# Kernel optimization log

Measured on AMD Instinct MI355X. Metric: run time of the kernel, lower is better.

Reference implementation:

```python
import jax, jax.numpy as jnp
import numpy as np

VOCAB = 50257
K = 10  # accuracy_slack_size


def setup_inputs() -> dict:
    key = jax.random.key(0)
    k1, k2, k3, k4 = jax.random.split(key, 4)
    logits = jax.random.normal(k1, (4, 2048, 512), dtype=jnp.float32)
    target = jax.random.randint(k2, (4, 2048), 0, VOCAB, dtype=jnp.int64 if jax.config.jax_enable_x64 else jnp.int32)
    mask = jax.random.randint(k3, (4, 2048), 0, 2, dtype=jnp.int32)
    W = jax.random.normal(k4, (512, VOCAB), dtype=jnp.float32) * 0.02
    b = jnp.zeros((VOCAB,), dtype=jnp.float32)
    return {"logits": logits, "target": target, "mask": mask, "W": W, "b": b}


def reference(logits, target, mask, W, b):
    N = logits.shape[0] * logits.shape[1]
    x = logits.reshape(N, logits.shape[-1])            # [N, d]
    # sampled_softmax.log_prob: full log-softmax over vocab
    logp = jax.nn.log_softmax(x @ W + b, axis=-1)      # [N, V]
    _, words = jax.lax.top_k(logp, K)                  # [N, K] indices
    tgt = target.reshape(-1)                           # [N]
    msk = mask.reshape(-1).astype(jnp.float32)         # [N]
    # vectorized membership: is target among top-K predictions?
    hit = jnp.any(words == tgt[:, None], axis=1).astype(jnp.float32)
    counter = jnp.sum(hit * msk)
    all_counter = jnp.sum(msk)
    return jnp.array([counter / all_counter])
```

## Files before the change

### kernel.cpp

```cpp
#include <hip/hip_runtime.h>
#include <stdint.h>

#define V_VOCAB 50257
#define V_PAD   51200
#define NROWS   8192
#define DIM     512
#define KTOP    10
#define ACH     16

typedef __attribute__((ext_vector_type(8))) short  short8;
typedef __attribute__((ext_vector_type(4))) float  f32x4;
typedef __attribute__((ext_vector_type(4))) int    i32x4;
typedef __attribute__((ext_vector_type(2))) unsigned int u32x2;

struct Ctrl { int mc; int namb; int hits; int pad_; };

#define OFF_WT8    0ULL
#define SZ_WT8     26214400ULL
#define OFF_XQ8    (OFF_WT8 + SZ_WT8)
#define SZ_XQ8     4194304ULL
#define OFF_BPAD   (OFF_XQ8 + SZ_XQ8)
#define SZ_COL     (51200ULL*4)
#define OFF_SW8    (OFF_BPAD + SZ_COL)
#define OFF_W1     (OFF_SW8 + SZ_COL)
#define OFF_IVW    (OFF_W1 + SZ_COL)
#define OFF_ROWIDX (OFF_IVW + SZ_COL)
#define OFF_SXR    (OFF_ROWIDX + 32768ULL)
#define OFF_X1     (OFF_SXR + 32768ULL)
#define OFF_THAT   (OFF_X1 + 32768ULL)
#define OFF_ETG    (OFF_THAT + 32768ULL)
#define OFF_COUNTS (OFF_ETG + 32768ULL)
#define OFF_AMB    (OFF_COUNTS + 32768ULL)
#define OFF_CTRL   (OFF_AMB + 32768ULL)
#define OFF_RK     (OFF_CTRL + 16ULL)
#define OFF_SST    (OFF_RK + 32768ULL)

#define GLOAD16(gp, lp) __builtin_amdgcn_global_load_lds( \
    (const __attribute__((address_space(1))) unsigned int*)(gp), \
    (__attribute__((address_space(3))) unsigned int*)(lp), 16, 0, 0)

__global__ void k_prep(const int* __restrict__ mask, const float* __restrict__ b,
                       float* __restrict__ bpad, int* __restrict__ rowidx,
                       Ctrl* __restrict__ ctrl) {
  int i = blockIdx.x * 256 + threadIdx.x;
  if (i < V_PAD) bpad[i] = (i < V_VOCAB) ? b[i] : -1e30f;
  if (i < NROWS && mask[i] != 0) {
    int p = atomicAdd(&ctrl->mc, 1);
    rowidx[p] = i;
  }
}

__global__ void k_wstat(const float* __restrict__ W, float* __restrict__ sw8,
                        float* __restrict__ w1, float* __restrict__ invw) {
  const int j = blockIdx.x * 256 + threadIdx.x;
  if (j >= V_PAD) return;
  if (j >= V_VOCAB) { sw8[j] = 1.f; w1[j] = 0.f; invw[j] = 0.f; return; }
  float am = 0.f, s1 = 0.f;
  for (int k = 0; k < DIM; ++k) {
    float v = fabsf(W[(size_t)k * V_VOCAB + j]);
    am = fmaxf(am, v);
    s1 += v;
  }
  sw8[j] = (am > 0.f) ? am / 126.f : 1.f;
  invw[j] = (am > 0.f) ? 126.f / am : 0.f;
  w1[j] = s1;
}

__global__ void k_twt8(const float* __restrict__ W, const float* __restrict__ invw,
                       signed char* __restrict__ Wt8) {
  __shared__ float lt[64][65];
  const int vbase = blockIdx.x * 64;
  const int kbase = blockIdx.y * 64;
  const int tid = threadIdx.x;
  const int krow = tid >> 6;
  const int col  = tid & 63;
  const int v    = vbase + col;
#pragma unroll
  for (int rr = 0; rr < 16; ++rr) {
    int kl = krow + rr * 4;
    float val = (v < V_VOCAB) ? W[(size_t)(kbase + kl) * V_VOCAB + v] : 0.0f;
    lt[kl][col] = val;
  }
  __syncthreads();
  const int vr = tid >> 3;
  const int kc = tid & 7;
#pragma unroll
  for (int p = 0; p < 2; ++p) {
    const int vl = p * 32 + vr;
    const float inv = invw[vbase + vl];
    unsigned int lo = 0, hi = 0;
#pragma unroll
    for (int j = 0; j < 4; ++j) {
      int q = (int)rintf(lt[kc * 8 + j][vl] * inv);
      lo |= ((unsigned int)(q & 255)) << (8 * j);
    }
#pragma unroll
    for (int j = 0; j < 4; ++j) {
      int q = (int)rintf(lt[kc * 8 + 4 + j][vl] * inv);
      hi |= ((unsigned int)(q & 255)) << (8 * j);
    }
    u32x2 t; t.x = lo; t.y = hi;
    *(u32x2*)(Wt8 + (size_t)(vbase + vl) * DIM + kbase + kc * 8) = t;
  }
}

__global__ void k_xq(const float* __restrict__ x, const int* __restrict__ rowidx,
                     const Ctrl* __restrict__ ctrl, signed char* __restrict__ Xq8,
                     float* __restrict__ sxr, float* __restrict__ x1) {
  const int wid = threadIdx.x >> 6, lane = threadIdx.x & 63;
  const int i = blockIdx.x * 4 + wid;
  const int mc = ctrl->mc;
  if (i >= mc) {
    u32x2 z; z.x = 0; z.y = 0;
    *(u32x2*)(Xq8 + (size_t)i * DIM + lane * 8) = z;
    if (lane == 0) { sxr[i] = 1.f; x1[i] = 0.f; }
    return;
  }
  const float* src = x + (size_t)rowidx[i] * DIM + lane * 8;
  float v[8];
  float am = 0.f, s1 = 0.f;
#pragma unroll
  for (int j = 0; j < 8; ++j) {
    v[j] = src[j];
    float a = fabsf(v[j]);
    am = fmaxf(am, a);
    s1 += a;
  }
#pragma unroll
  for (int d = 1; d < 64; d <<= 1) {
    am = fmaxf(am, __shfl_xor(am, d, 64));
    s1 += __shfl_xor(s1, d, 64);
  }
  const float sx  = (am > 0.f) ? am / 126.f : 1.f;
  const float inv = (am > 0.f) ? 126.f / am : 0.f;
  unsigned int lo = 0, hi = 0;
#pragma unroll
  for (int j = 0; j < 4; ++j) {
    int q = (int)rintf(v[j] * inv);
    lo |= ((unsigned int)(q & 255)) << (8 * j);
  }
#pragma unroll
  for (int j = 0; j < 4; ++j) {
    int q = (int)rintf(v[4 + j] * inv);
    hi |= ((unsigned int)(q & 255)) << (8 * j);
  }
  u32x2 t; t.x = lo; t.y = hi;
  *(u32x2*)(Xq8 + (size_t)i * DIM + lane * 8) = t;
  if (lane == 0) { sxr[i] = sx; x1[i] = s1; }
}

__global__ void k_that8(const signed char* __restrict__ Xq8,
                        const signed char* __restrict__ Wt8,
                        const float* __restrict__ bpad, const float* __restrict__ sw8,
                        const float* __restrict__ w1,
                        const float* __restrict__ sxr, const float* __restrict__ x1,
                        const int* __restrict__ rowidx, const int* __restrict__ target,
                        const Ctrl* __restrict__ ctrl, float* __restrict__ that,
                        float* __restrict__ etg) {
  const int wid = threadIdx.x >> 6, lane = threadIdx.x & 63;
  const int i = blockIdx.x * 4 + wid;
  const int mc = ctrl->mc;
  if (i >= mc) { if (lane == 0) { that[i] = 1e30f; etg[i] = 0.f; } return; }
  const int tg = target[rowidx[i]];
  u32x2 xq = *(const u32x2*)(Xq8 + (size_t)i * DIM + lane * 8);
  u32x2 wq = *(const u32x2*)(Wt8 + (size_t)tg * DIM + lane * 8);
  int d = 0;
#pragma unroll
  for (int j = 0; j < 4; ++j)
    d += (int)((signed char)(xq.x >> (8 * j))) * (int)((signed char)(wq.x >> (8 * j)));
#pragma unroll
  for (int j = 0; j < 4; ++j)
    d += (int)((signed char)(xq.y >> (8 * j))) * (int)((signed char)(wq.y >> (8 * j)));
#pragma unroll
  for (int dd = 1; dd < 64; dd <<= 1) d += __shfl_xor(d, dd, 64);
  if (lane == 0) {
    const float sx = sxr[i], sw = sw8[tg];
    that[i] = fmaf((float)d, sx * sw, bpad[tg]);
    etg[i] = 0.5005f * (sx * w1[tg] + sw * x1[i]) + 128.5f * (sx * sw);
  }
}

__launch_bounds__(256, 2)
__global__ void k_count8(const signed char* __restrict__ Xq8,
                         const signed char* __restrict__ Wt8,
                         const float* __restrict__ bpad, const float* __restrict__ sw8,
                         const float* __restrict__ w1, const float* __restrict__ sxr,
                         const float* __restrict__ x1, const float* __restrict__ that,
                         const float* __restrict__ etg,
                         const Ctrl* __restrict__ ctrl, unsigned int* __restrict__ counts) {
  const int mc = ctrl->mc;
  const int lin = blockIdx.x;
  const int xcd = lin & 7;
  const int idx = lin >> 3;
  const int mt  = xcd * 4 + (idx & 3);
  const int nt  = idx >> 2;
  const int mbase = mt * 128;
  if (mbase >= mc) return;
  const int nbase = nt * 128;

  __shared__ char lds[65536];

  const int tid  = threadIdx.x;
  const int lane = tid & 63;
  const int w    = tid >> 6;
  const int wr   = w >> 1;
  const int wc   = w & 1;

  const char* Ag = (const char*)Xq8 + (size_t)mbase * 512;
  const char* Bg = (const char*)Wt8 + (size_t)nbase * 512;
  const int r8   = tid >> 3;
  const int sws  = ((tid & 7) ^ (r8 & 7)) * 16;
  const int dst0 = tid * 16;

  const int fr = lane & 15;
  const int fq = lane >> 4;
  const int p0 = ((fq) ^ (fr & 7)) * 16;
  const int p1 = ((4 + fq) ^ (fr & 7)) * 16;

#define STAGE(q, kt) do {                                                      \
    const size_t _kb = (size_t)(kt) * 128;                                     \
    _Pragma("unroll") for (int _c = 0; _c < 4; ++_c)                           \
      GLOAD16(Ag + (size_t)(_c * 32 + r8) * 512 + _kb + sws,                   \
              lds + (q) * 32768 + _c * 4096 + dst0);                           \
    _Pragma("unroll") for (int _c = 0; _c < 4; ++_c)                           \
      GLOAD16(Bg + (size_t)(_c * 32 + r8) * 512 + _kb + sws,                   \
              lds + (q) * 32768 + 16384 + _c * 4096 + dst0);                   \
  } while (0)

  i32x4 acc[4][4];
#pragma unroll
  for (int a = 0; a < 4; ++a)
#pragma unroll
    for (int c = 0; c < 4; ++c) acc[a][c] = (i32x4)0;

#define KTILE(q) do {                                                          \
    const char* _ab = lds + (q) * 32768;                                       \
    const char* _bb = _ab + 16384;                                             \
    _Pragma("unroll") for (int _ks = 0; _ks < 2; ++_ks) {                      \
      const int _p = _ks ? p1 : p0;                                            \
      i32x4 a4[4], b4[4];                                                      \
      _Pragma("unroll") for (int _i = 0; _i < 4; ++_i)                         \
        a4[_i] = *(const i32x4*)(_ab + (wr * 64 + _i * 16 + fr) * 128 + _p);   \
      _Pragma("unroll") for (int _i = 0; _i < 4; ++_i)                         \
        b4[_i] = *(const i32x4*)(_bb + (wc * 64 + _i * 16 + fr) * 128 + _p);   \
      __builtin_amdgcn_s_setprio(1);                                           \
      _Pragma("unroll") for (int _m = 0; _m < 4; ++_m)                         \
      _Pragma("unroll") for (int _n = 0; _n < 4; ++_n)                         \
        acc[_m][_n] = __builtin_amdgcn_mfma_i32_16x16x64_i8(                   \
            a4[_m], b4[_n], acc[_m][_n], 0, 0, 0);                             \
      __builtin_amdgcn_s_setprio(0);                                           \
    }                                                                          \
  } while (0)

  STAGE(0, 0);
  __syncthreads();
#pragma unroll
  for (int kt = 0; kt < 4; ++kt) {
    if (kt < 3) STAGE((kt + 1) & 1, kt + 1);
    KTILE(kt & 1);
    __syncthreads();
  }

  float bv[4], swc[4], w1c[4];
#pragma unroll
  for (int ni = 0; ni < 4; ++ni) {
    const int c = nbase + wc * 64 + ni * 16 + fr;
    bv[ni] = bpad[c]; swc[ni] = sw8[c]; w1c[ni] = w1[c];
  }

#pragma unroll
  for (int mi = 0; mi < 4; ++mi) {
#pragma unroll
    for (int r = 0; r < 4; ++r) {
      const int m = mbase + wr * 64 + mi * 16 + fq * 4 + r;
      const float sx = sxr[m], x1r = x1[m], th = that[m], eg = etg[m];
      unsigned int p = 0;
#pragma unroll
      for (int ni = 0; ni < 4; ++ni) {
        const float scl = sx * swc[ni];
        const float s = fmaf((float)acc[mi][ni][r], scl, bv[ni]);
        const float mm = 0.5005f * (sx * w1c[ni] + swc[ni] * x1r)
                         + 128.5f * scl + eg + 1e-3f;
        p += (s > th - mm) ? 1u : 0u;
        p += (s > th + mm) ? (1u << 16) : 0u;
      }
      int pi = (int)p;
#pragma unroll
      for (int d = 1; d < 16; d <<= 1) pi += __shfl_xor(pi, d, 64);
      if ((lane & 15) == 0) atomicAdd(&counts[m], (unsigned int)pi);
    }
  }
#undef STAGE
#undef KTILE
}

__global__ void k_decide(const unsigned int* __restrict__ counts,
                         Ctrl* __restrict__ ctrl, int* __restrict__ amb) {
  const int i = blockIdx.x * 256 + threadIdx.x;
  if (i >= ctrl->mc) return;
  const unsigned int c = counts[i];
  const unsigned int lo = c & 0xFFFFu, hi = c >> 16;
  if (lo <= KTOP - 1) { atomicAdd(&ctrl->hits, 1); }
  else if (hi >= KTOP) {  }
  else { int p = atomicAdd(&ctrl->namb, 1); amb[p] = i; }
}

__global__ void k_fixt(const float* __restrict__ x, const float* __restrict__ W,
                       const float* __restrict__ b, const int* __restrict__ rowidx,
                       const int* __restrict__ target, const int* __restrict__ amb,
                       const Ctrl* __restrict__ ctrl, float* __restrict__ sst) {
  const int a = blockIdx.x * 64 + threadIdx.x;
  if (a >= ctrl->namb) return;
  const int n = rowidx[amb[a]];
  const int tg = target[n];
  float st = 0.f;
  for (int k = 0; k < DIM; ++k)
    st = fmaf(x[(size_t)n * DIM + k], W[(size_t)k * V_VOCAB + tg], st);
  sst[a] = st + b[tg];
}

__global__ void k_fixscan(const float* __restrict__ x, const float* __restrict__ W,
                          const float* __restrict__ b, const int* __restrict__ rowidx,
                          const int* __restrict__ target, const int* __restrict__ amb,
                          const float* __restrict__ sst, const Ctrl* __restrict__ ctrl,
                          int* __restrict__ rk) {
  __shared__ float sx[ACH][DIM];
  const int j = blockIdx.x * 256 + threadIdx.x;
  const int namb = ctrl->namb;
  const float bj = (j < V_VOCAB) ? b[j] : 0.f;
  for (int base = 0; base < namb; base += ACH) {
    __syncthreads();
    for (int t = threadIdx.x; t < ACH * DIM / 4; t += 256) {
      const int a  = t / (DIM / 4);
      const int kk = (t % (DIM / 4)) * 4;
      f32x4 v = (f32x4)0.f;
      if (base + a < namb) {
        const int n = rowidx[amb[base + a]];
        v = *(const f32x4*)(x + (size_t)n * DIM + kk);
      }
      *(f32x4*)(&sx[a][kk]) = v;
    }
    __syncthreads();
    if (j >= V_VOCAB) continue;
    float s[ACH];
#pragma unroll
    for (int a = 0; a < ACH; ++a) s[a] = 0.f;
    for (int k = 0; k < DIM; ++k) {
      const float wv = W[(size_t)k * V_VOCAB + j];
#pragma unroll
      for (int a = 0; a < ACH; ++a) s[a] = fmaf(sx[a][k], wv, s[a]);
    }
#pragma unroll
    for (int a = 0; a < ACH; ++a) {
      if (base + a < namb) {
        const int tg = target[rowidx[amb[base + a]]];
        const float sc = s[a] + bj;
        const float st = sst[base + a];
        if (sc > st || (sc == st && j < tg)) atomicAdd(&rk[base + a], 1);
      }
    }
  }
}

__global__ void k_fixdec(const int* __restrict__ rk, Ctrl* __restrict__ ctrl) {
  const int a = blockIdx.x * 256 + threadIdx.x;
  if (a < ctrl->namb && rk[a] <= KTOP - 1) atomicAdd(&ctrl->hits, 1);
}

__global__ void k_final(const Ctrl* __restrict__ ctrl, float* __restrict__ out) {
  out[0] = (float)ctrl->hits / (float)ctrl->mc;
}

extern "C" void kernel_launch(void* const* d_in, const int* in_sizes, int n_in,
                              void* d_out, int out_size, void* d_ws, size_t ws_size,
                              hipStream_t stream) {
  const float* x      = (const float*)d_in[0];
  const int*   target = (const int*)d_in[1];
  const int*   mask   = (const int*)d_in[2];
  const float* W      = (const float*)d_in[3];
  const float* b      = (const float*)d_in[4];
  float* out = (float*)d_out;

  char* ws = (char*)d_ws;
  signed char*    Wt8    = (signed char*)(ws + OFF_WT8);
  signed char*    Xq8    = (signed char*)(ws + OFF_XQ8);
  float*          bpad   = (float*)(ws + OFF_BPAD);
  float*          sw8    = (float*)(ws + OFF_SW8);
  float*          w1     = (float*)(ws + OFF_W1);
  float*          invw   = (float*)(ws + OFF_IVW);
  int*            rowidx = (int*)(ws + OFF_ROWIDX);
  float*          sxr    = (float*)(ws + OFF_SXR);
  float*          x1     = (float*)(ws + OFF_X1);
  float*          that   = (float*)(ws + OFF_THAT);
  float*          etg    = (float*)(ws + OFF_ETG);
  unsigned int*   counts = (unsigned int*)(ws + OFF_COUNTS);
  int*            amb    = (int*)(ws + OFF_AMB);
  Ctrl*           ctrl   = (Ctrl*)(ws + OFF_CTRL);
  int*            rk     = (int*)(ws + OFF_RK);
  float*          sst    = (float*)(ws + OFF_SST);

  hipMemsetAsync(ws + OFF_COUNTS, 0, 32768 + 32768 + 16 + 32768, stream);

  k_prep   <<<200, 256, 0, stream>>>(mask, b, bpad, rowidx, ctrl);
  k_wstat  <<<200, 256, 0, stream>>>(W, sw8, w1, invw);
  k_twt8   <<<dim3(800, 8), 256, 0, stream>>>(W, invw, Wt8);
  k_xq     <<<2048, 256, 0, stream>>>(x, rowidx, ctrl, Xq8, sxr, x1);
  k_that8  <<<2048, 256, 0, stream>>>(Xq8, Wt8, bpad, sw8, w1, sxr, x1,
                                      rowidx, target, ctrl, that, etg);
  k_count8 <<<12800, 256, 0, stream>>>(Xq8, Wt8, bpad, sw8, w1, sxr, x1,
                                       that, etg, ctrl, counts);
  k_decide <<<32, 256, 0, stream>>>(counts, ctrl, amb);
  k_fixt   <<<128, 64, 0, stream>>>(x, W, b, rowidx, target, amb, ctrl, sst);
  k_fixscan<<<197, 256, 0, stream>>>(x, W, b, rowidx, target, amb, sst, ctrl, rk);
  k_fixdec <<<32, 256, 0, stream>>>(rk, ctrl);
  k_final  <<<1, 1, 0, stream>>>(ctrl, out);
}
```

Before: 494.0 us.

## Single-buffer LDS, pack per-row metadata, loop M tiles for higher occupancy

The int8 counting GEMM drops its double-buffered 64KB LDS for a single 32KB buffer and raises launch bounds from 2 to 5 blocks per CU. Blocks whose row tile fell beyond the masked-row count used to exit immediately; now each block loops over M tiles with a stride of 4096 rows. Per-row scale, threshold and margin terms are precomputed into one float4 so the epilogue does a single vector load and fewer FLOPs. Giving up the prefetch overlap between tiles is traded for more resident waves to hide latency, and the tighter register budget risks spills.

Result: slower. 715.6 us (+44.9%).

```diff
diff --git a/kernel.cpp b/kernel.cpp
--- a/kernel.cpp
+++ b/kernel.cpp
@@ -27,9 +27,8 @@
 #define OFF_ROWIDX (OFF_IVW + SZ_COL)
 #define OFF_SXR    (OFF_ROWIDX + 32768ULL)
 #define OFF_X1     (OFF_SXR + 32768ULL)
-#define OFF_THAT   (OFF_X1 + 32768ULL)
-#define OFF_ETG    (OFF_THAT + 32768ULL)
-#define OFF_COUNTS (OFF_ETG + 32768ULL)
+#define OFF_RMETA  (OFF_X1 + 32768ULL)
+#define OFF_COUNTS (OFF_RMETA + 131072ULL)
 #define OFF_AMB    (OFF_COUNTS + 32768ULL)
 #define OFF_CTRL   (OFF_AMB + 32768ULL)
 #define OFF_RK     (OFF_CTRL + 16ULL)
@@ -155,12 +154,14 @@
                         const float* __restrict__ w1,
                         const float* __restrict__ sxr, const float* __restrict__ x1,
                         const int* __restrict__ rowidx, const int* __restrict__ target,
-                        const Ctrl* __restrict__ ctrl, float* __restrict__ that,
-                        float* __restrict__ etg) {
+                        const Ctrl* __restrict__ ctrl, f32x4* __restrict__ rmeta) {
   const int wid = threadIdx.x >> 6, lane = threadIdx.x & 63;
   const int i = blockIdx.x * 4 + wid;
   const int mc = ctrl->mc;
-  if (i >= mc) { if (lane == 0) { that[i] = 1e30f; etg[i] = 0.f; } return; }
+  if (i >= mc) {
+    if (lane == 0) { f32x4 rm; rm.x = 1.f; rm.y = 1e30f; rm.z = 0.f; rm.w = 0.f; rmeta[i] = rm; }
+    return;
+  }
   const int tg = target[rowidx[i]];
   u32x2 xq = *(const u32x2*)(Xq8 + (size_t)i * DIM + lane * 8);
   u32x2 wq = *(const u32x2*)(Wt8 + (size_t)tg * DIM + lane * 8);
@@ -174,19 +175,22 @@
 #pragma unroll
   for (int dd = 1; dd < 64; dd <<= 1) d += __shfl_xor(d, dd, 64);
   if (lane == 0) {
-    const float sx = sxr[i], sw = sw8[tg];
-    that[i] = fmaf((float)d, sx * sw, bpad[tg]);
-    etg[i] = 0.5005f * (sx * w1[tg] + sw * x1[i]) + 128.5f * (sx * sw);
-  }
-}
-
-__launch_bounds__(256, 2)
+    const float sx = sxr[i], sw = sw8[tg], xl1 = x1[i];
+    f32x4 rm;
+    rm.x = sx;
+    rm.y = fmaf((float)d, sx * sw, bpad[tg]);
+    rm.z = 0.5005f * (sx * w1[tg] + sw * xl1) + 128.5f * (sx * sw)
+           + 1e-3f;
+    rm.w = fmaf(128.5f, sx, 0.5005f * xl1);
+    rmeta[i] = rm;
+  }
+}
+
+__launch_bounds__(256, 5)
 __global__ void k_count8(const signed char* __restrict__ Xq8,
                          const signed char* __restrict__ Wt8,
                          const float* __restrict__ bpad, const float* __restrict__ sw8,
-                         const float* __restrict__ w1, const float* __restrict__ sxr,
-                         const float* __restrict__ x1, const float* __restrict__ that,
-                         const float* __restrict__ etg,
+                         const float* __restrict__ w1, const f32x4* __restrict__ rmeta,
                          const Ctrl* __restrict__ ctrl, unsigned int* __restrict__ counts) {
   const int mc = ctrl->mc;
   const int lin = blockIdx.x;
@@ -194,11 +198,9 @@
   const int idx = lin >> 3;
   const int mt  = xcd * 4 + (idx & 3);
   const int nt  = idx >> 2;
-  const int mbase = mt * 128;
-  if (mbase >= mc) return;
   const int nbase = nt * 128;
 
-  __shared__ char lds[65536];
+  __shared__ char lds[32768];
 
   const int tid  = threadIdx.x;
   const int lane = tid & 63;
@@ -206,7 +208,6 @@
   const int wr   = w >> 1;
   const int wc   = w & 1;
 
-  const char* Ag = (const char*)Xq8 + (size_t)mbase * 512;
   const char* Bg = (const char*)Wt8 + (size_t)nbase * 512;
   const int r8   = tid >> 3;
   const int sws  = ((tid & 7) ^ (r8 & 7)) * 16;
@@ -217,32 +218,25 @@
   const int p0 = ((fq) ^ (fr & 7)) * 16;
   const int p1 = ((4 + fq) ^ (fr & 7)) * 16;
 
-#define STAGE(q, kt) do {                                                      \
+#define STAGE(Ag, kt) do {                                                     \
     const size_t _kb = (size_t)(kt) * 128;                                     \
     _Pragma("unroll") for (int _c = 0; _c < 4; ++_c)                           \
-      GLOAD16(Ag + (size_t)(_c * 32 + r8) * 512 + _kb + sws,                   \
-              lds + (q) * 32768 + _c * 4096 + dst0);                           \
+      GLOAD16((Ag) + (size_t)(_c * 32 + r8) * 512 + _kb + sws,                 \
+              lds + _c * 4096 + dst0);                                         \
     _Pragma("unroll") for (int _c = 0; _c < 4; ++_c)                           \
       GLOAD16(Bg + (size_t)(_c * 32 + r8) * 512 + _kb + sws,                   \
-              lds + (q) * 32768 + 16384 + _c * 4096 + dst0);                   \
+              lds + 16384 + _c * 4096 + dst0);                                 \
   } while (0)
 
-  i32x4 acc[4][4];
-#pragma unroll
-  for (int a = 0; a < 4; ++a)
-#pragma unroll
-    for (int c = 0; c < 4; ++c) acc[a][c] = (i32x4)0;
-
-#define KTILE(q) do {                                                          \
-    const char* _ab = lds + (q) * 32768;                                       \
-    const char* _bb = _ab + 16384;                                             \
+#define KTILE() do {                                                           \
     _Pragma("unroll") for (int _ks = 0; _ks < 2; ++_ks) {                      \
       const int _p = _ks ? p1 : p0;                                            \
       i32x4 a4[4], b4[4];                                                      \
       _Pragma("unroll") for (int _i = 0; _i < 4; ++_i)                         \
-        a4[_i] = *(const i32x4*)(_ab + (wr * 64 + _i * 16 + fr) * 128 + _p);   \
+        a4[_i] = *(const i32x4*)(lds + (wr * 64 + _i * 16 + fr) * 128 + _p);   \
       _Pragma("unroll") for (int _i = 0; _i < 4; ++_i)                         \
-        b4[_i] = *(const i32x4*)(_bb + (wc * 64 + _i * 16 + fr) * 128 + _p);   \
+        b4[_i] = *(const i32x4*)(lds + 16384 +                                 \
+                                 (wc * 64 + _i * 16 + fr) * 128 + _p);         \
       __builtin_amdgcn_s_setprio(1);                                           \
       _Pragma("unroll") for (int _m = 0; _m < 4; ++_m)                         \
       _Pragma("unroll") for (int _n = 0; _n < 4; ++_n)                         \
@@ -252,14 +246,7 @@
     }                                                                          \
   } while (0)
 
-  STAGE(0, 0);
-  __syncthreads();
-#pragma unroll
-  for (int kt = 0; kt < 4; ++kt) {
-    if (kt < 3) STAGE((kt + 1) & 1, kt + 1);
-    KTILE(kt & 1);
-    __syncthreads();
-  }
+  i32x4 acc[4][4];
 
   float bv[4], swc[4], w1c[4];
 #pragma unroll
@@ -268,26 +255,41 @@
     bv[ni] = bpad[c]; swc[ni] = sw8[c]; w1c[ni] = w1[c];
   }
 
-#pragma unroll
-  for (int mi = 0; mi < 4; ++mi) {
-#pragma unroll
-    for (int r = 0; r < 4; ++r) {
-      const int m = mbase + wr * 64 + mi * 16 + fq * 4 + r;
-      const float sx = sxr[m], x1r = x1[m], th = that[m], eg = etg[m];
-      unsigned int p = 0;
-#pragma unroll
-      for (int ni = 0; ni < 4; ++ni) {
-        const float scl = sx * swc[ni];
-        const float s = fmaf((float)acc[mi][ni][r], scl, bv[ni]);
-        const float mm = 0.5005f * (sx * w1c[ni] + swc[ni] * x1r)
-                         + 128.5f * scl + eg + 1e-3f;
-        p += (s > th - mm) ? 1u : 0u;
-        p += (s > th + mm) ? (1u << 16) : 0u;
+  for (int mb = mt * 128; mb < mc; mb += 4096) {
+    const char* Ag = (const char*)Xq8 + (size_t)mb * 512;
+#pragma unroll
+    for (int a = 0; a < 4; ++a)
+#pragma unroll
+      for (int c = 0; c < 4; ++c) acc[a][c] = (i32x4)0;
+
+#pragma unroll
+    for (int kt = 0; kt < 4; ++kt) {
+      STAGE(Ag, kt);
+      __syncthreads();
+      KTILE();
+      __syncthreads();
+    }
+
+#pragma unroll
+    for (int mi = 0; mi < 4; ++mi) {
+#pragma unroll
+      for (int r = 0; r < 4; ++r) {
+        const int m = mb + wr * 64 + mi * 16 + fq * 4 + r;
+        const f32x4 rm = rmeta[m];
+        const float arr = 0.5005f * rm.x;
+        unsigned int p = 0;
+#pragma unroll
+        for (int ni = 0; ni < 4; ++ni) {
+          const float s  = fmaf((float)acc[mi][ni][r], rm.x * swc[ni], bv[ni]);
+          const float mm = fmaf(arr, w1c[ni], fmaf(rm.w, swc[ni], rm.z));
+          p += (s > rm.y - mm) ? 1u : 0u;
+          p += (s > rm.y + mm) ? (1u << 16) : 0u;
+        }
+        int pi = (int)p;
+#pragma unroll
+        for (int d = 1; d < 16; d <<= 1) pi += __shfl_xor(pi, d, 64);
+        if ((lane & 15) == 0) atomicAdd(&counts[m], (unsigned int)pi);
       }
-      int pi = (int)p;
-#pragma unroll
-      for (int d = 1; d < 16; d <<= 1) pi += __shfl_xor(pi, d, 64);
-      if ((lane & 15) == 0) atomicAdd(&counts[m], (unsigned int)pi);
     }
   }
 #undef STAGE
@@ -391,8 +393,7 @@
   int*            rowidx = (int*)(ws + OFF_ROWIDX);
   float*          sxr    = (float*)(ws + OFF_SXR);
   float*          x1     = (float*)(ws + OFF_X1);
-  float*          that   = (float*)(ws + OFF_THAT);
-  float*          etg    = (float*)(ws + OFF_ETG);
+  f32x4*          rmeta  = (f32x4*)(ws + OFF_RMETA);
   unsigned int*   counts = (unsigned int*)(ws + OFF_COUNTS);
   int*            amb    = (int*)(ws + OFF_AMB);
   Ctrl*           ctrl   = (Ctrl*)(ws + OFF_CTRL);
@@ -406,9 +407,9 @@
   k_twt8   <<<dim3(800, 8), 256, 0, stream>>>(W, invw, Wt8);
   k_xq     <<<2048, 256, 0, stream>>>(x, rowidx, ctrl, Xq8, sxr, x1);
   k_that8  <<<2048, 256, 0, stream>>>(Xq8, Wt8, bpad, sw8, w1, sxr, x1,
-                                      rowidx, target, ctrl, that, etg);
-  k_count8 <<<12800, 256, 0, stream>>>(Xq8, Wt8, bpad, sw8, w1, sxr, x1,
-                                       that, etg, ctrl, counts);
+                                      rowidx, target, ctrl, rmeta);
+  k_count8 <<<12800, 256, 0, stream>>>(Xq8, Wt8, bpad, sw8, w1, rmeta,
+                                       ctrl, counts);
   k_decide <<<32, 256, 0, stream>>>(counts, ctrl, amb);
   k_fixt   <<<128, 64, 0, stream>>>(x, W, b, rowidx, target, amb, ctrl, sst);
   k_fixscan<<<197, 256, 0, stream>>>(x, W, b, rowidx, target, amb, sst, ctrl, rk);
```
